# Performance work log

Measured on AMD Instinct MI355X. Metric: run time of the kernel, lower is better.

## Reference

```python
import jax, jax.numpy as jnp
import numpy as np


def setup_inputs() -> dict:
    key = jax.random.key(0)
    ks = jax.random.split(key, 9)
    b, h, w, c = 32, 64, 64, 256
    s = 0.02  # small init to mimic variance-scaled NIN weights
    return {
        "x": jax.random.normal(ks[0], (b, h, w, c), dtype=jnp.float32),
        "Wq": jax.random.normal(ks[1], (c, c), dtype=jnp.float32) * s,
        "bq": jnp.zeros((c,), dtype=jnp.float32),
        "Wk": jax.random.normal(ks[2], (c, c), dtype=jnp.float32) * s,
        "bk": jnp.zeros((c,), dtype=jnp.float32),
        "Wv": jax.random.normal(ks[3], (c, c), dtype=jnp.float32) * s,
        "bv": jnp.zeros((c,), dtype=jnp.float32),
        "Wo": jax.random.normal(ks[4], (c, c), dtype=jnp.float32) * s,
        "bo": jnp.zeros((c,), dtype=jnp.float32),
    }


def reference(x, Wq, bq, Wk, bk, Wv, bv, Wo, bo):
    # x: [b, h, w, c]. NOTE: in the source, GroupNorm(x) is computed but its
    # output is immediately overwritten (dead code); Q/K/V come from raw x.
    b, h, w, c = x.shape
    cf = jnp.asarray(c, x.dtype)
    Q = jnp.einsum('bhwc,cd->bhwd', x, Wq) + bq
    K = jnp.einsum('bhwc,cd->bhwd', x, Wk) + bk
    V = jnp.einsum('bhwc,cd->bhwd', x, Wv) + bv
    # per-row attention over the W axis: scores [b, h, w, w]
    # double scaling: /(c*sqrt(1/2)) then softmax(./sqrt(c))
    scores = jnp.einsum('bhic,bhjc->bhij', Q, K) / (cf * jnp.sqrt(jnp.asarray(0.5, x.dtype)))
    attn = jax.nn.softmax(scores / jnp.sqrt(cf), axis=-1)
    out = jnp.einsum('bhij,bhjc->bhic', attn, V)
    out = jnp.einsum('bhwc,cd->bhwd', out, Wo) + bo
    return out + x
```

## Files before the change

kernel.cpp:

```cpp
#include <hip/hip_runtime.h>
#include <hip/hip_bf16.h>
#include <stdint.h>


typedef __bf16 bf16x8 __attribute__((ext_vector_type(8)));
typedef __bf16 bf16x4 __attribute__((ext_vector_type(4)));
typedef float f32x4 __attribute__((ext_vector_type(4)));

#define C 256
#define WTOK 64
#define CP 264
#define PP 72

__device__ float  g_wT[3 * 65536];
__device__ __bf16 g_wqk[65536];
__device__ __bf16 g_wvo[65536];
__device__ float  g_c[256];
__device__ float  g_bvo[256];

__device__ __forceinline__ bf16x8 ld8(const __bf16* p) {
  return *reinterpret_cast<const bf16x8*>(p);
}

__global__ __launch_bounds__(256) void trans_kernel(
    const float* __restrict__ wq, const float* __restrict__ wk,
    const float* __restrict__ wv) {
  __shared__ float tile[32][33];
  const float* src = (blockIdx.z == 0) ? wq : (blockIdx.z == 1) ? wk : wv;
  float* d = &g_wT[0] + (size_t)blockIdx.z * 65536;
  const int tx = threadIdx.x, ty = threadIdx.y;
  const int k0 = blockIdx.x * 32;
  const int m0 = blockIdx.y * 32;
  for (int i = 0; i < 4; ++i)
    tile[ty + 8 * i][tx] = src[(size_t)(k0 + ty + 8 * i) * 256 + m0 + tx];
  __syncthreads();
  for (int i = 0; i < 4; ++i)
    d[(size_t)(m0 + ty + 8 * i) * 256 + k0 + tx] = tile[tx][ty + 8 * i];
}

__global__ __launch_bounds__(256) void fold_kernel(
    const float* __restrict__ wk, const float* __restrict__ wo) {
  const int n = blockIdx.x;
  const int k = threadIdx.x;
  float acc = 0.f;
  if (blockIdx.y == 0) {
    const float* a = &g_wT[0];
    #pragma unroll 8
    for (int m = 0; m < 256; ++m) acc += a[m * 256 + k] * wk[n * 256 + m];
    g_wqk[n * 256 + k] = (__bf16)acc;
  } else {
    const float* a = &g_wT[2 * 65536];
    #pragma unroll 8
    for (int m = 0; m < 256; ++m) acc += a[m * 256 + k] * wo[m * 256 + n];
    g_wvo[n * 256 + k] = (__bf16)acc;
  }
}

__global__ __launch_bounds__(256) void bias_kernel(
    const float* __restrict__ bq, const float* __restrict__ bv,
    const float* __restrict__ bo, const float* __restrict__ wo) {
  const int n = threadIdx.x;
  const float* wkT = &g_wT[65536];
  float c = 0.f, bb = bo[n];
  #pragma unroll 8
  for (int m = 0; m < 256; ++m) c += bq[m] * wkT[m * 256 + n];
  #pragma unroll 8
  for (int k = 0; k < 256; ++k) bb += bv[k] * wo[k * 256 + n];
  g_c[n] = c;
  g_bvo[n] = bb;
}

__global__ __launch_bounds__(256, 2) void attn_fused_kernel(
    const float* __restrict__ x, float* __restrict__ out) {
  __shared__ __align__(16) __bf16 smem[38400];
  __bf16* xs = smem;
  __bf16* ts = smem + 16896;
  __bf16* ys = ts;
  __bf16* ps = smem + 33792;

  const int tid = threadIdx.x;
  const int wv = tid >> 6;
  const int lane = tid & 63;
  const int quad = lane >> 4;
  const int l16 = lane & 15;
  const int bh = blockIdx.x;
  const float* xrow = x + (size_t)bh * (WTOK * C);

  for (int it = 0; it < 16; ++it) {
    const int chunk = tid + it * 256;
    const int row = chunk >> 6;
    const int c4 = (chunk & 63) << 2;
    const float4 v = *reinterpret_cast<const float4*>(xrow + row * 256 + c4);
    bf16x4 b;
    b[0] = (__bf16)v.x; b[1] = (__bf16)v.y; b[2] = (__bf16)v.z; b[3] = (__bf16)v.w;
    *reinterpret_cast<bf16x4*>(xs + row * CP + c4) = b;
  }
  __syncthreads();

  const int nb = wv * 64;
  const int i0 = wv * 16;

  {
    f32x4 D[4][4];
    const f32x4 zero = {0.f, 0.f, 0.f, 0.f};
    for (int m = 0; m < 4; ++m)
      for (int nt = 0; nt < 4; ++nt) D[m][nt] = zero;
    for (int kc = 0; kc < 8; ++kc) {
      const int ko = kc * 32 + quad * 8;
      bf16x8 a[4];
      for (int m = 0; m < 4; ++m) a[m] = ld8(xs + (m * 16 + l16) * CP + ko);
      for (int nt = 0; nt < 4; ++nt) {
        bf16x8 b = ld8(g_wqk + (size_t)(nb + nt * 16 + l16) * 256 + ko);
        for (int m = 0; m < 4; ++m)
          D[m][nt] = __builtin_amdgcn_mfma_f32_16x16x32_bf16(a[m], b, D[m][nt], 0, 0, 0);
      }
    }
    float cs[4];
    for (int nt = 0; nt < 4; ++nt) cs[nt] = g_c[nb + nt * 16 + l16];
    for (int m = 0; m < 4; ++m)
      for (int nt = 0; nt < 4; ++nt)
        for (int r = 0; r < 4; ++r)
          ts[(m * 16 + quad * 4 + r) * CP + nb + nt * 16 + l16] =
              (__bf16)(D[m][nt][r] + cs[nt]);
  }
  __syncthreads();

  f32x4 S[4];
  {
    const f32x4 zero = {0.f, 0.f, 0.f, 0.f};
    for (int nt = 0; nt < 4; ++nt) S[nt] = zero;
    bf16x8 qa[8];
    for (int kc = 0; kc < 8; ++kc)
      qa[kc] = ld8(ts + (i0 + l16) * CP + kc * 32 + quad * 8);
    for (int nt = 0; nt < 4; ++nt)
      for (int kc = 0; kc < 8; ++kc) {
        bf16x8 kb = ld8(xs + (nt * 16 + l16) * CP + kc * 32 + quad * 8);
        S[nt] = __builtin_amdgcn_mfma_f32_16x16x32_bf16(qa[kc], kb, S[nt], 0, 0, 0);
      }
  }

  const float SCALE = 1.0f / (256.0f * 16.0f * 0.70710678118654752f);
  for (int r = 0; r < 4; ++r) {
    float p[4];
    float mx = -1e30f;
    for (int nt = 0; nt < 4; ++nt) {
      p[nt] = S[nt][r] * SCALE;
      mx = fmaxf(mx, p[nt]);
    }
    for (int msk = 1; msk < 16; msk <<= 1) mx = fmaxf(mx, __shfl_xor(mx, msk));
    float sum = 0.f;
    for (int nt = 0; nt < 4; ++nt) {
      p[nt] = __expf(p[nt] - mx);
      sum += p[nt];
    }
    for (int msk = 1; msk < 16; msk <<= 1) sum += __shfl_xor(sum, msk);
    const float invs = 1.0f / sum;
    for (int nt = 0; nt < 4; ++nt)
      ps[(i0 + quad * 4 + r) * PP + nt * 16 + l16] = (__bf16)(p[nt] * invs);
  }
  __syncthreads();

  {
    f32x4 Y[16];
    const f32x4 zero = {0.f, 0.f, 0.f, 0.f};
    for (int ct = 0; ct < 16; ++ct) Y[ct] = zero;
    bf16x8 pa[2];
    for (int kc = 0; kc < 2; ++kc)
      pa[kc] = ld8(ps + (i0 + l16) * PP + kc * 32 + quad * 8);
    for (int ct = 0; ct < 16; ++ct) {
      const int ch = ct * 16 + l16;
      for (int kc = 0; kc < 2; ++kc) {
        bf16x8 xb;
        #pragma unroll
        for (int jj = 0; jj < 8; ++jj) {
          const int j = kc * 32 + quad * 8 + jj;
          xb[jj] = (__bf16)xrow[j * 256 + ch];
        }
        Y[ct] = __builtin_amdgcn_mfma_f32_16x16x32_bf16(pa[kc], xb, Y[ct], 0, 0, 0);
      }
    }
    for (int ct = 0; ct < 16; ++ct)
      for (int r = 0; r < 4; ++r)
        ys[(i0 + quad * 4 + r) * CP + ct * 16 + l16] = (__bf16)Y[ct][r];
  }
  __syncthreads();

  {
    f32x4 D[4][4];
    const f32x4 zero = {0.f, 0.f, 0.f, 0.f};
    for (int m = 0; m < 4; ++m)
      for (int nt = 0; nt < 4; ++nt) D[m][nt] = zero;
    for (int kc = 0; kc < 8; ++kc) {
      const int ko = kc * 32 + quad * 8;
      bf16x8 a[4];
      for (int m = 0; m < 4; ++m) a[m] = ld8(ys + (m * 16 + l16) * CP + ko);
      for (int nt = 0; nt < 4; ++nt) {
        bf16x8 b = ld8(g_wvo + (size_t)(nb + nt * 16 + l16) * 256 + ko);
        for (int m = 0; m < 4; ++m)
          D[m][nt] = __builtin_amdgcn_mfma_f32_16x16x32_bf16(a[m], b, D[m][nt], 0, 0, 0);
      }
    }
    float bs[4];
    for (int nt = 0; nt < 4; ++nt) bs[nt] = g_bvo[nb + nt * 16 + l16];
    for (int m = 0; m < 4; ++m)
      for (int nt = 0; nt < 4; ++nt)
        for (int r = 0; r < 4; ++r) {
          const int tok = m * 16 + quad * 4 + r;
          const int ch = nb + nt * 16 + l16;
          out[((size_t)bh * WTOK + tok) * C + ch] =
              D[m][nt][r] + bs[nt] + xrow[tok * 256 + ch];
        }
  }
}

extern "C" void kernel_launch(void* const* d_in, const int* in_sizes, int n_in,
                              void* d_out, int out_size, void* d_ws, size_t ws_size,
                              hipStream_t stream) {
  (void)in_sizes; (void)n_in; (void)out_size; (void)d_ws; (void)ws_size;
  const float* x  = (const float*)d_in[0];
  const float* Wq = (const float*)d_in[1];
  const float* bq = (const float*)d_in[2];
  const float* Wk = (const float*)d_in[3];
  const float* Wv = (const float*)d_in[5];
  const float* bv = (const float*)d_in[6];
  const float* Wo = (const float*)d_in[7];
  const float* bo = (const float*)d_in[8];
  float* out = (float*)d_out;

  hipLaunchKernelGGL(trans_kernel, dim3(8, 8, 3), dim3(32, 8, 1), 0, stream, Wq, Wk, Wv);
  hipLaunchKernelGGL(fold_kernel, dim3(256, 2, 1), dim3(256), 0, stream, Wk, Wo);
  hipLaunchKernelGGL(bias_kernel, dim3(1), dim3(256), 0, stream, bq, bv, bo, Wo);
  hipLaunchKernelGGL(attn_fused_kernel, dim3(2048), dim3(256), 0, stream, x, out);
}
```

Baseline: 381.6 us.

## Reorder attention to project V through Wvo before the P·V product

```diff
diff --git a/kernel.cpp b/kernel.cpp
--- a/kernel.cpp
+++ b/kernel.cpp
@@ -10,6 +10,7 @@
 #define C 256
 #define WTOK 64
 #define CP 264
+#define VP 72
 #define PP 72
 
 __device__ float  g_wT[3 * 65536];
@@ -72,11 +73,11 @@
 
 __global__ __launch_bounds__(256, 2) void attn_fused_kernel(
     const float* __restrict__ x, float* __restrict__ out) {
-  __shared__ __align__(16) __bf16 smem[38400];
+  __shared__ __align__(16) __bf16 smem[39936];
   __bf16* xs = smem;
   __bf16* ts = smem + 16896;
-  __bf16* ys = ts;
-  __bf16* ps = smem + 33792;
+  __bf16* vt = ts;
+  __bf16* ps = smem + 35328;
 
   const int tid = threadIdx.x;
   const int wv = tid >> 6;
@@ -160,32 +161,17 @@
   }
   __syncthreads();
 
-  {
-    f32x4 Y[16];
-    const f32x4 zero = {0.f, 0.f, 0.f, 0.f};
-    for (int ct = 0; ct < 16; ++ct) Y[ct] = zero;
-    bf16x8 pa[2];
-    for (int kc = 0; kc < 2; ++kc)
-      pa[kc] = ld8(ps + (i0 + l16) * PP + kc * 32 + quad * 8);
-    for (int ct = 0; ct < 16; ++ct) {
-      const int ch = ct * 16 + l16;
-      for (int kc = 0; kc < 2; ++kc) {
-        bf16x8 xb;
-        #pragma unroll
-        for (int jj = 0; jj < 8; ++jj) {
-          const int j = kc * 32 + quad * 8 + jj;
-          xb[jj] = (__bf16)xrow[j * 256 + ch];
-        }
-        Y[ct] = __builtin_amdgcn_mfma_f32_16x16x32_bf16(pa[kc], xb, Y[ct], 0, 0, 0);
-      }
-    }
+  float xres[64];
+  float bvo[16];
+  {
+    #pragma unroll
+    for (int ct = 0; ct < 16; ++ct) bvo[ct] = g_bvo[ct * 16 + l16];
+    #pragma unroll
     for (int ct = 0; ct < 16; ++ct)
+      #pragma unroll
       for (int r = 0; r < 4; ++r)
-        ys[(i0 + quad * 4 + r) * CP + ct * 16 + l16] = (__bf16)Y[ct][r];
-  }
-  __syncthreads();
-
-  {
+        xres[ct * 4 + r] = xrow[(i0 + quad * 4 + r) * 256 + ct * 16 + l16];
+
     f32x4 D[4][4];
     const f32x4 zero = {0.f, 0.f, 0.f, 0.f};
     for (int m = 0; m < 4; ++m)
@@ -193,23 +179,48 @@
     for (int kc = 0; kc < 8; ++kc) {
       const int ko = kc * 32 + quad * 8;
       bf16x8 a[4];
-      for (int m = 0; m < 4; ++m) a[m] = ld8(ys + (m * 16 + l16) * CP + ko);
+      for (int m = 0; m < 4; ++m) a[m] = ld8(xs + (m * 16 + l16) * CP + ko);
       for (int nt = 0; nt < 4; ++nt) {
         bf16x8 b = ld8(g_wvo + (size_t)(nb + nt * 16 + l16) * 256 + ko);
         for (int m = 0; m < 4; ++m)
           D[m][nt] = __builtin_amdgcn_mfma_f32_16x16x32_bf16(a[m], b, D[m][nt], 0, 0, 0);
       }
     }
-    float bs[4];
-    for (int nt = 0; nt < 4; ++nt) bs[nt] = g_bvo[nb + nt * 16 + l16];
-    for (int m = 0; m < 4; ++m)
-      for (int nt = 0; nt < 4; ++nt)
-        for (int r = 0; r < 4; ++r) {
-          const int tok = m * 16 + quad * 4 + r;
-          const int ch = nb + nt * 16 + l16;
-          out[((size_t)bh * WTOK + tok) * C + ch] =
-              D[m][nt][r] + bs[nt] + xrow[tok * 256 + ch];
-        }
+    for (int nt = 0; nt < 4; ++nt) {
+      const int ch = nb + nt * 16 + l16;
+      for (int m = 0; m < 4; ++m) {
+        bf16x4 v4;
+        for (int r = 0; r < 4; ++r) v4[r] = (__bf16)D[m][nt][r];
+        *reinterpret_cast<bf16x4*>(vt + ch * VP + m * 16 + quad * 4) = v4;
+      }
+    }
+  }
+  __syncthreads();
+
+  {
+    f32x4 Y[16];
+    const f32x4 zero = {0.f, 0.f, 0.f, 0.f};
+    for (int ct = 0; ct < 16; ++ct) Y[ct] = zero;
+    bf16x8 pa[2];
+    for (int kc = 0; kc < 2; ++kc)
+      pa[kc] = ld8(ps + (i0 + l16) * PP + kc * 32 + quad * 8);
+    #pragma unroll
+    for (int ct = 0; ct < 16; ++ct) {
+      #pragma unroll
+      for (int kc = 0; kc < 2; ++kc) {
+        bf16x8 vb = ld8(vt + (ct * 16 + l16) * VP + kc * 32 + quad * 8);
+        Y[ct] = __builtin_amdgcn_mfma_f32_16x16x32_bf16(pa[kc], vb, Y[ct], 0, 0, 0);
+      }
+    }
+    #pragma unroll
+    for (int ct = 0; ct < 16; ++ct) {
+      const int ch = ct * 16 + l16;
+      #pragma unroll
+      for (int r = 0; r < 4; ++r) {
+        const int tok = i0 + quad * 4 + r;
+        out[((size_t)bh * WTOK + tok) * C + ch] = Y[ct][r] + bvo[ct] + xres[ct * 4 + r];
+      }
+    }
   }
 }
 
```

Result: faster. 358.5 us (-6.1%).
